# Optimization experiments

Measured on AMD Instinct MI355X. Metric: run time of the kernel, lower is better.

The kernel has to match this reference:

```python
import jax, jax.numpy as jnp
import numpy as np

B, T, D = 4, 4096, 512

def setup_inputs() -> dict:
    key = jax.random.key(0)
    k1, k2, k3 = jax.random.split(key, 3)
    z_hat = jax.random.normal(k1, (B, T, D), dtype=jnp.float32)
    P = jax.random.uniform(k2, (B, T), dtype=jnp.float32)
    lengths = jax.random.randint(k3, (B,), 0, T).astype(jnp.int32)
    return {"z_hat": z_hat, "P": P, "lengths": lengths}

def reference(z_hat, P, lengths):
    # z_hat: [B, T, D], P: [B, T], lengths: [B]
    Bs, Tc, _ = z_hat.shape
    P_clamped = jnp.clip(P, 0.0, 1.0 - 1e-6)
    q = 1.0 - P_clamped
    # inclusive cumulative sum of log q (same as padded-cumsum[:,1:] in torch)
    log_cumprod_q = jnp.cumsum(jnp.log(q), axis=1)                 # [B, T]
    log_P = jnp.log(jnp.clip(P_clamped, 1e-6, None))               # [B, T]
    # log_M[b, t, k] = log P[b, k] + logcum[b, t] - logcum[b, k], causal (k <= t)
    log_M = (log_P[:, None, :]
             + log_cumprod_q[:, :, None]
             - log_cumprod_q[:, None, :])                          # [B, T, T]
    t_idx = jnp.arange(Tc)
    causal = t_idx[:, None] >= t_idx[None, :]                      # k <= t kept
    M = jnp.where(causal[None, :, :], jnp.exp(log_M), 0.0)         # [B, T, T]
    z_bar = jnp.einsum('btk,bkd->btd', M, z_hat)                   # [B, T, D]
    padding_mask = t_idx[None, :] < lengths[:, None]               # [B, T]
    return z_bar * padding_mask[:, :, None].astype(z_bar.dtype)
```

## Files before the change

kernel.cpp:

```cpp
#include <hip/hip_runtime.h>


#define CHUNK 64
#define MAX_NC 512

__global__ __launch_bounds__(512) void k_local(
    const float* __restrict__ z, const float* __restrict__ P,
    float* __restrict__ S, float* __restrict__ A,
    int B, int T, int D, int NC) {
  int blk = blockIdx.x;
  int b = blk / NC, c = blk % NC;
  int t0 = c * CHUNK;
  __shared__ float p_s[CHUNK], q_s[CHUNK];
  int tid = threadIdx.x;
  if (tid < CHUNK) {
    int tg = t0 + tid;
    float p = (tg < T) ? P[(size_t)b * T + tg] : 0.0f;
    p = fminf(fmaxf(p, 0.0f), 1.0f - 1e-6f);
    q_s[tid] = 1.0f - p;
    p_s[tid] = fmaxf(p, 1e-6f);
  }
  __syncthreads();
  int nt = min(CHUNK, T - t0);
  for (int d = tid; d < D; d += blockDim.x) {
    const float* zp = z + ((size_t)b * T + t0) * D + d;
    float s = 0.0f, r = 1.0f;
    for (int t = 0; t < nt; ++t) {
      s = fmaf(q_s[t], s, p_s[t] * zp[(size_t)t * D]);
      r *= q_s[t];
    }
    S[((size_t)b * NC + c) * D + d] = s;
    if (d == 0) A[b * NC + c] = r;
  }
}

__global__ __launch_bounds__(512) void k_apply(
    const float* __restrict__ z, const float* __restrict__ P,
    const float* __restrict__ S, const float* __restrict__ A,
    const int* __restrict__ lengths, float* __restrict__ out,
    int B, int T, int D, int NC) {
  int blk = blockIdx.x;
  int b = blk / NC, c = blk % NC;
  int t0 = c * CHUNK;
  __shared__ float p_s[CHUNK], q_s[CHUNK];
  __shared__ float a_s[MAX_NC];
  int tid = threadIdx.x;
  if (tid < CHUNK) {
    int tg = t0 + tid;
    float p = (tg < T) ? P[(size_t)b * T + tg] : 0.0f;
    p = fminf(fmaxf(p, 0.0f), 1.0f - 1e-6f);
    q_s[tid] = 1.0f - p;
    p_s[tid] = fmaxf(p, 1e-6f);
  }
  for (int i = tid; i < NC; i += blockDim.x) a_s[i] = A[b * NC + i];
  __syncthreads();
  int L = lengths[b];
  int nt = min(CHUNK, T - t0);
  for (int d = tid; d < D; d += blockDim.x) {
    float carry = 0.0f, w = 1.0f;
    for (int cp = c - 1; cp >= 0; --cp) {
      carry = fmaf(S[((size_t)b * NC + cp) * D + d], w, carry);
      w *= a_s[cp];
    }
    const float* zp = z + ((size_t)b * T + t0) * D + d;
    float* op = out + ((size_t)b * T + t0) * D + d;
    float s = carry;
    for (int t = 0; t < nt; ++t) {
      s = fmaf(q_s[t], s, p_s[t] * zp[(size_t)t * D]);
      op[(size_t)t * D] = ((t0 + t) < L) ? s : 0.0f;
    }
  }
}

extern "C" void kernel_launch(void* const* d_in, const int* in_sizes, int n_in,
                              void* d_out, int out_size, void* d_ws, size_t ws_size,
                              hipStream_t stream) {
  const float* z = (const float*)d_in[0];
  const float* P = (const float*)d_in[1];
  const int* lengths = (const int*)d_in[2];
  float* out = (float*)d_out;

  int B = in_sizes[2];
  int T = in_sizes[1] / B;
  int D = in_sizes[0] / in_sizes[1];
  int NC = (T + CHUNK - 1) / CHUNK;

  float* S = (float*)d_ws;
  float* A = S + (size_t)B * NC * D;

  dim3 grid(B * NC), block(512);
  k_local<<<grid, block, 0, stream>>>(z, P, S, A, B, T, D, NC);
  k_apply<<<grid, block, 0, stream>>>(z, P, S, A, lengths, out, B, T, D, NC);
}
```

Baseline: 97.57 us.

## Vectorize chunked scan with float4, shrink chunks, skip chunks beyond sequence length

Both kernels now process four channels per thread with float4 loads and stores, and use 128-thread blocks with chunks of 32 timesteps. Chunks that start at or past lengths[b] skip the local scan entirely, and the apply kernel only writes zeros for them. This avoids reading z for padded positions. Full chunks get an unrolled fast path without per-element masking. Smaller chunks double the number of chunk summaries, so the serial carry loop over previous chunks gets longer.

Measured after the change: 99.70 us. 1.02x slower.

```diff
diff --git a/kernel.cpp b/kernel.cpp
--- a/kernel.cpp
+++ b/kernel.cpp
@@ -1,16 +1,20 @@
 #include <hip/hip_runtime.h>
 
 
-#define CHUNK 64
+#define CHUNK 32
+#define BLOCK 128
 #define MAX_NC 512
 
-__global__ __launch_bounds__(512) void k_local(
+__global__ __launch_bounds__(BLOCK) void k_local(
     const float* __restrict__ z, const float* __restrict__ P,
-    float* __restrict__ S, float* __restrict__ A,
+    const int* __restrict__ lengths,
+    float4* __restrict__ S, float* __restrict__ A,
     int B, int T, int D, int NC) {
   int blk = blockIdx.x;
   int b = blk / NC, c = blk % NC;
   int t0 = c * CHUNK;
+  if (t0 >= lengths[b]) return;
+
   __shared__ float p_s[CHUNK], q_s[CHUNK];
   int tid = threadIdx.x;
   if (tid < CHUNK) {
@@ -21,30 +25,63 @@
     p_s[tid] = fmaxf(p, 1e-6f);
   }
   __syncthreads();
+
   int nt = min(CHUNK, T - t0);
-  for (int d = tid; d < D; d += blockDim.x) {
-    const float* zp = z + ((size_t)b * T + t0) * D + d;
-    float s = 0.0f, r = 1.0f;
-    for (int t = 0; t < nt; ++t) {
-      s = fmaf(q_s[t], s, p_s[t] * zp[(size_t)t * D]);
-      r *= q_s[t];
+  int D4 = D >> 2;
+  const float4* zp = (const float4*)z + ((size_t)b * T + t0) * D4;
+  for (int d4 = tid; d4 < D4; d4 += BLOCK) {
+    float4 s = make_float4(0.f, 0.f, 0.f, 0.f);
+    float r = 1.0f;
+    if (nt == CHUNK) {
+#pragma unroll
+      for (int t = 0; t < CHUNK; ++t) {
+        float4 zv = zp[(size_t)t * D4 + d4];
+        float q = q_s[t], pe = p_s[t];
+        s.x = fmaf(q, s.x, pe * zv.x);
+        s.y = fmaf(q, s.y, pe * zv.y);
+        s.z = fmaf(q, s.z, pe * zv.z);
+        s.w = fmaf(q, s.w, pe * zv.w);
+        r *= q;
+      }
+    } else {
+      for (int t = 0; t < nt; ++t) {
+        float4 zv = zp[(size_t)t * D4 + d4];
+        float q = q_s[t], pe = p_s[t];
+        s.x = fmaf(q, s.x, pe * zv.x);
+        s.y = fmaf(q, s.y, pe * zv.y);
+        s.z = fmaf(q, s.z, pe * zv.z);
+        s.w = fmaf(q, s.w, pe * zv.w);
+        r *= q;
+      }
     }
-    S[((size_t)b * NC + c) * D + d] = s;
-    if (d == 0) A[b * NC + c] = r;
+    S[((size_t)b * NC + c) * D4 + d4] = s;
+    if (d4 == 0) A[b * NC + c] = r;
   }
 }
 
-__global__ __launch_bounds__(512) void k_apply(
+__global__ __launch_bounds__(BLOCK) void k_apply(
     const float* __restrict__ z, const float* __restrict__ P,
-    const float* __restrict__ S, const float* __restrict__ A,
+    const float4* __restrict__ S, const float* __restrict__ A,
     const int* __restrict__ lengths, float* __restrict__ out,
     int B, int T, int D, int NC) {
   int blk = blockIdx.x;
   int b = blk / NC, c = blk % NC;
   int t0 = c * CHUNK;
+  int tid = threadIdx.x;
+  int L = lengths[b];
+  int nt = min(CHUNK, T - t0);
+  int D4 = D >> 2;
+  float4* op = (float4*)out + ((size_t)b * T + t0) * D4;
+
+  if (t0 >= L) {
+    float4 zero = make_float4(0.f, 0.f, 0.f, 0.f);
+    for (int d4 = tid; d4 < D4; d4 += BLOCK)
+      for (int t = 0; t < nt; ++t) op[(size_t)t * D4 + d4] = zero;
+    return;
+  }
+
   __shared__ float p_s[CHUNK], q_s[CHUNK];
   __shared__ float a_s[MAX_NC];
-  int tid = threadIdx.x;
   if (tid < CHUNK) {
     int tg = t0 + tid;
     float p = (tg < T) ? P[(size_t)b * T + tg] : 0.0f;
@@ -52,22 +89,44 @@
     q_s[tid] = 1.0f - p;
     p_s[tid] = fmaxf(p, 1e-6f);
   }
-  for (int i = tid; i < NC; i += blockDim.x) a_s[i] = A[b * NC + i];
+  for (int i = tid; i < c; i += BLOCK) a_s[i] = A[b * NC + i];
   __syncthreads();
-  int L = lengths[b];
-  int nt = min(CHUNK, T - t0);
-  for (int d = tid; d < D; d += blockDim.x) {
-    float carry = 0.0f, w = 1.0f;
+
+  const float4* Sb = S + (size_t)b * NC * D4;
+  const float4* zp = (const float4*)z + ((size_t)b * T + t0) * D4;
+  for (int d4 = tid; d4 < D4; d4 += BLOCK) {
+    float4 s = make_float4(0.f, 0.f, 0.f, 0.f);
+    float w = 1.0f;
     for (int cp = c - 1; cp >= 0; --cp) {
-      carry = fmaf(S[((size_t)b * NC + cp) * D + d], w, carry);
+      float4 sv = Sb[(size_t)cp * D4 + d4];
+      s.x = fmaf(sv.x, w, s.x);
+      s.y = fmaf(sv.y, w, s.y);
+      s.z = fmaf(sv.z, w, s.z);
+      s.w = fmaf(sv.w, w, s.w);
       w *= a_s[cp];
     }
-    const float* zp = z + ((size_t)b * T + t0) * D + d;
-    float* op = out + ((size_t)b * T + t0) * D + d;
-    float s = carry;
-    for (int t = 0; t < nt; ++t) {
-      s = fmaf(q_s[t], s, p_s[t] * zp[(size_t)t * D]);
-      op[(size_t)t * D] = ((t0 + t) < L) ? s : 0.0f;
+    if (nt == CHUNK && t0 + CHUNK <= L) {
+#pragma unroll
+      for (int t = 0; t < CHUNK; ++t) {
+        float4 zv = zp[(size_t)t * D4 + d4];
+        float q = q_s[t], pe = p_s[t];
+        s.x = fmaf(q, s.x, pe * zv.x);
+        s.y = fmaf(q, s.y, pe * zv.y);
+        s.z = fmaf(q, s.z, pe * zv.z);
+        s.w = fmaf(q, s.w, pe * zv.w);
+        op[(size_t)t * D4 + d4] = s;
+      }
+    } else {
+      float4 zero = make_float4(0.f, 0.f, 0.f, 0.f);
+      for (int t = 0; t < nt; ++t) {
+        float4 zv = zp[(size_t)t * D4 + d4];
+        float q = q_s[t], pe = p_s[t];
+        s.x = fmaf(q, s.x, pe * zv.x);
+        s.y = fmaf(q, s.y, pe * zv.y);
+        s.z = fmaf(q, s.z, pe * zv.z);
+        s.w = fmaf(q, s.w, pe * zv.w);
+        op[(size_t)t * D4 + d4] = ((t0 + t) < L) ? s : zero;
+      }
     }
   }
 }
@@ -85,10 +144,10 @@
   int D = in_sizes[0] / in_sizes[1];
   int NC = (T + CHUNK - 1) / CHUNK;
 
-  float* S = (float*)d_ws;
-  float* A = S + (size_t)B * NC * D;
+  float4* S = (float4*)d_ws;
+  float* A = (float*)d_ws + (size_t)B * NC * D;
 
-  dim3 grid(B * NC), block(512);
-  k_local<<<grid, block, 0, stream>>>(z, P, S, A, B, T, D, NC);
+  dim3 grid(B * NC), block(BLOCK);
+  k_local<<<grid, block, 0, stream>>>(z, P, lengths, S, A, B, T, D, NC);
   k_apply<<<grid, block, 0, stream>>>(z, P, S, A, lengths, out, B, T, D, NC);
 }
```
